# Performance work log

Hardware: AMD Instinct MI355X
Metric: run time of the kernel (lower is better)

The kernel has to match this reference:

```python
import jax, jax.numpy as jnp
import numpy as np

B, D, H = 4096, 1024, 1024


def setup_inputs() -> dict:
    key = jax.random.key(0)
    ks = jax.random.split(key, 20)
    s_in = 1.0 / np.sqrt(D)
    s_hid = 1.0 / np.sqrt(H)
    inp = {
        "x_t": jax.random.normal(ks[0], (B, D), dtype=jnp.float32),
        "h_t_1": jax.random.normal(ks[1], (B, H), dtype=jnp.float32),
        "c_t_1": jax.random.normal(ks[2], (B, H), dtype=jnp.float32),
        # input-to-hidden weights (nn.Linear: y = x @ W.T + b), stacked i,f,o,z
        "W": jax.random.uniform(ks[3], (4, H, D), minval=-s_in, maxval=s_in, dtype=jnp.float32),
        "bW": jax.random.uniform(ks[4], (4, H), minval=-s_in, maxval=s_in, dtype=jnp.float32),
        # hidden-to-hidden weights, stacked i,f,o,z
        "U": jax.random.uniform(ks[5], (4, H, H), minval=-s_hid, maxval=s_hid, dtype=jnp.float32),
        "bU": jax.random.uniform(ks[6], (4, H), minval=-s_hid, maxval=s_hid, dtype=jnp.float32),
    }
    return inp


def reference(x_t, h_t_1, c_t_1, W, bW, U, bU):
    # Two stacked GEMMs: [B,D]x[4,H,D] -> [4,B,H], [B,H]x[4,H,H] -> [4,B,H]
    gx = jnp.einsum("bd,ghd->gbh", x_t, W) + bW[:, None, :]
    gh = jnp.einsum("bh,gkh->gbk", h_t_1, U) + bU[:, None, :]
    g = gx + gh  # [4, B, H] pre-activations for i, f, o, z
    i = jax.nn.sigmoid(g[0])
    f = jax.nn.sigmoid(g[1])
    o = jax.nn.sigmoid(g[2])
    z = jnp.tanh(g[3])
    c_t = i * z + f * c_t_1
    h_t = o * jnp.tanh(c_t)
    return (h_t, c_t)
```

## Files before the change

kernel.cpp:

```cpp
#include <hip/hip_runtime.h>
#include <math.h>

#define Mm 4096
#define Nn 4096
#define Kk 2048

typedef __bf16 bf16x8 __attribute__((ext_vector_type(8)));
typedef float f32x4 __attribute__((ext_vector_type(4)));

__device__ __forceinline__ unsigned short f2bf(float f) {
    union { float f; unsigned u; } v; v.f = f;
    unsigned r = v.u + 0x7FFFu + ((v.u >> 16) & 1u);
    return (unsigned short)(r >> 16);
}

__device__ __forceinline__ float fast_tanh(float x) {
    return 1.f - 2.f / (1.f + __expf(2.f * x));
}

__global__ void pack_bf16(const float* __restrict__ x, const float* __restrict__ h,
                          const float* __restrict__ W, const float* __restrict__ U,
                          const float* __restrict__ bW, const float* __restrict__ bU,
                          unsigned short* __restrict__ Xc, unsigned short* __restrict__ Wc,
                          float* __restrict__ bsum) {
    if (blockIdx.x == 0) {
#pragma unroll
        for (int j = 0; j < 16; ++j) {
            int n = threadIdx.x * 16 + j;
            int hh = n >> 2, g = n & 3;
            bsum[n] = bW[g * 1024 + hh] + bU[g * 1024 + hh];
        }
    }
    const int PER = (4096 * 1024) / 4;
    for (int t = blockIdx.x * blockDim.x + threadIdx.x; t < 4 * PER;
         t += gridDim.x * blockDim.x) {
        int region = t >> 20;
        int i = t & (PER - 1);
        int row = i >> 8;
        int c4  = i & 255;
        const float* src = (region == 0) ? x : (region == 1) ? h : (region == 2) ? W : U;
        float4 v = reinterpret_cast<const float4*>(src)[i];
        ushort4 o;
        o.x = f2bf(v.x); o.y = f2bf(v.y); o.z = f2bf(v.z); o.w = f2bf(v.w);
        if (region < 2) {
            *reinterpret_cast<ushort4*>(Xc + (size_t)row * 2048 + (region << 10) + c4 * 4) = o;
        } else {
            int g = row >> 10, hh = row & 1023;
            int np = ((hh >> 4) << 6) + (g << 4) + (hh & 15);
            *reinterpret_cast<ushort4*>(Wc + (size_t)np * 2048 + ((region & 1) << 10) + c4 * 4) = o;
        }
    }
}

__device__ __forceinline__ void gl16(const void* g, void* l) {
    __builtin_amdgcn_global_load_lds(
        (const __attribute__((address_space(1))) void*)g,
        (__attribute__((address_space(3))) void*)l, 16, 0, 0);
}

#define A_OFF(p, ah) (((p) * 2 + (ah)) * 16384)
#define B_OFF(p, hb) (65536 + ((p) * 2 + (hb)) * 16384)

__global__ __launch_bounds__(512, 2) void gemm_8ph(const unsigned short* __restrict__ A,
                                                   const unsigned short* __restrict__ Bw,
                                                   const float* __restrict__ bsum,
                                                   const float* __restrict__ cprev,
                                                   float* __restrict__ out) {
    extern __shared__ char lds[];
    const int tid = threadIdx.x, lane = tid & 63, wave = tid >> 6;
    const int wm = wave >> 2, wn = wave & 3;

    const int bid = blockIdx.x;
    const int swz = (bid & 7) * 32 + (bid >> 3);
    const int bm = swz & 15, bn = swz >> 4;
    const size_t Crow0 = (size_t)bm * 256, Ccol0 = (size_t)bn * 256;

    const int srow = wave * 8 + (lane >> 3);
    const int scolswz = (((lane & 7) ^ (lane >> 3)) << 4);
    const char* aS[2][2];
    const char* bS[2][2];
#pragma unroll
    for (int ah = 0; ah < 2; ++ah)
#pragma unroll
        for (int j = 0; j < 2; ++j) {
            aS[ah][j] = (const char*)A  + (size_t)(Crow0 + ah * 128 + j * 64 + srow) * 4096 + scolswz;
            bS[ah][j] = (const char*)Bw + (size_t)(Ccol0 + ah * 128 + j * 64 + srow) * 4096 + scolswz;
        }

#define STG_A(p, ah, kb) do { \
        gl16(aS[ah][0] + (kb), lds + A_OFF(p, ah) + wave * 1024); \
        gl16(aS[ah][1] + (kb), lds + A_OFF(p, ah) + 8192 + wave * 1024); } while (0)
#define STG_B(p, hb, kb) do { \
        gl16(bS[hb][0] + (kb), lds + B_OFF(p, hb) + wave * 1024); \
        gl16(bS[hb][1] + (kb), lds + B_OFF(p, hb) + 8192 + wave * 1024); } while (0)

    const int arowB = (wm * 64 + (lane & 15)) * 128;
    const int browB = ((wn & 1) * 64 + (lane & 15)) * 128;
    const int c0 = (((lane >> 4) << 4)) ^ ((lane & 7) << 4);
    const int c1 = (64 + ((lane >> 4) << 4)) ^ ((lane & 7) << 4);
    const int bhb = wn >> 1;

#define LDA(p, ah, mfl, ck) (*(const bf16x8*)(lds + A_OFF(p, ah) + arowB + (mfl) * 2048 + (ck)))
#define LDB(p, nf, ck)      (*(const bf16x8*)(lds + B_OFF(p, bhb) + browB + (nf) * 2048 + (ck)))

    f32x4 acc[2][4][4] = {};

#define MFMA(a, b, c) __builtin_amdgcn_mfma_f32_16x16x32_bf16(a, b, c, 0, 0, 0)
#define MF16(ah, mfA, mfB, p00, p01, p10, p11) \
    acc[ah][mfA][0] = MFMA(p00, b00, acc[ah][mfA][0]); \
    acc[ah][mfA][1] = MFMA(p00, b10, acc[ah][mfA][1]); \
    acc[ah][mfA][2] = MFMA(p00, b20, acc[ah][mfA][2]); \
    acc[ah][mfA][3] = MFMA(p00, b30, acc[ah][mfA][3]); \
    acc[ah][mfB][0] = MFMA(p10, b00, acc[ah][mfB][0]); \
    acc[ah][mfB][1] = MFMA(p10, b10, acc[ah][mfB][1]); \
    acc[ah][mfB][2] = MFMA(p10, b20, acc[ah][mfB][2]); \
    acc[ah][mfB][3] = MFMA(p10, b30, acc[ah][mfB][3]); \
    acc[ah][mfA][0] = MFMA(p01, b01, acc[ah][mfA][0]); \
    acc[ah][mfA][1] = MFMA(p01, b11, acc[ah][mfA][1]); \
    acc[ah][mfA][2] = MFMA(p01, b21, acc[ah][mfA][2]); \
    acc[ah][mfA][3] = MFMA(p01, b31, acc[ah][mfA][3]); \
    acc[ah][mfB][0] = MFMA(p11, b01, acc[ah][mfB][0]); \
    acc[ah][mfB][1] = MFMA(p11, b11, acc[ah][mfB][1]); \
    acc[ah][mfB][2] = MFMA(p11, b21, acc[ah][mfB][2]); \
    acc[ah][mfB][3] = MFMA(p11, b31, acc[ah][mfB][3]);

#define SGB0 __builtin_amdgcn_sched_barrier(0)
#define SBAR __builtin_amdgcn_s_barrier()

#define GROUP(p, kbA1, kbT2) \
    { \
         \
        bf16x8 b00 = LDB(p, 0, c0), b01 = LDB(p, 0, c1), b10 = LDB(p, 1, c0), b11 = LDB(p, 1, c1); \
        bf16x8 b20 = LDB(p, 2, c0), b21 = LDB(p, 2, c1), b30 = LDB(p, 3, c0), b31 = LDB(p, 3, c1); \
        bf16x8 a0 = LDA(p, 0, 0, c0), a1 = LDA(p, 0, 0, c1); \
        bf16x8 a2 = LDA(p, 0, 1, c0), a3 = LDA(p, 0, 1, c1); \
        bf16x8 n0 = LDA(p, 0, 2, c0), n1 = LDA(p, 0, 2, c1); \
        bf16x8 n2 = LDA(p, 0, 3, c0), n3 = LDA(p, 0, 3, c1); \
        STG_A((p) ^ 1, 1, kbA1); \
        asm volatile("s_waitcnt vmcnt(6)" ::: "memory"); \
        SGB0; \
        __builtin_amdgcn_s_setprio(1); \
        MF16(0, 0, 1, a0, a1, a2, a3) \
        __builtin_amdgcn_s_setprio(0); \
        SBAR; \
         \
        a0 = LDA(p, 1, 0, c0); a1 = LDA(p, 1, 0, c1); \
        a2 = LDA(p, 1, 1, c0); a3 = LDA(p, 1, 1, c1); \
        STG_B(p, 0, kbT2); \
        asm volatile("s_waitcnt vmcnt(6)" ::: "memory"); \
        SGB0; \
        __builtin_amdgcn_s_setprio(1); \
        MF16(0, 2, 3, n0, n1, n2, n3) \
        __builtin_amdgcn_s_setprio(0); \
        SBAR; \
         \
        n0 = LDA(p, 1, 2, c0); n1 = LDA(p, 1, 2, c1); \
        n2 = LDA(p, 1, 3, c0); n3 = LDA(p, 1, 3, c1); \
        STG_A(p, 0, kbT2); \
        asm volatile("s_waitcnt vmcnt(6)" ::: "memory"); \
        SGB0; \
        __builtin_amdgcn_s_setprio(1); \
        MF16(1, 0, 1, a0, a1, a2, a3) \
        __builtin_amdgcn_s_setprio(0); \
        SBAR; \
         \
        STG_B(p, 1, kbT2); \
        SGB0; \
        __builtin_amdgcn_s_setprio(1); \
        MF16(1, 2, 3, n0, n1, n2, n3) \
        __builtin_amdgcn_s_setprio(0); \
        SBAR; \
    }

    STG_B(0, 0, 0);
    STG_A(0, 0, 0);
    STG_B(0, 1, 0);
    STG_A(0, 1, 0);
    STG_B(1, 0, 128);
    STG_A(1, 0, 128);
    STG_B(1, 1, 128);
    asm volatile("s_waitcnt vmcnt(6)" ::: "memory");
    __builtin_amdgcn_s_barrier();

    for (int it = 0; it < 16; ++it) {
        const int t0 = 2 * it;
        const size_t kA1_0 = (size_t)(t0 + 1) * 128;
        const size_t kT2_0 = (t0 + 2 <= 31) ? (size_t)(t0 + 2) * 128 : 0;
        const size_t kA1_1 = kT2_0;
        const size_t kT2_1 = (t0 + 3 <= 31) ? (size_t)(t0 + 3) * 128 : 0;
        GROUP(0, kA1_0, kT2_0)
        GROUP(1, kA1_1, kT2_1)
    }

    const int hl = lane & 15;
    const int er0 = (lane >> 4) * 4;
    const int myh = (int)(Ccol0 >> 2) + wn * 16 + hl;
    const f32x4 bs = *(const f32x4*)(bsum + (size_t)myh * 4);

    float cp[2][4][4];
#pragma unroll
    for (int ah = 0; ah < 2; ++ah)
#pragma unroll
        for (int mf = 0; mf < 4; ++mf)
#pragma unroll
            for (int r = 0; r < 4; ++r)
                cp[ah][mf][r] = cprev[(size_t)(Crow0 + ah * 128 + wm * 64 + mf * 16 + er0 + r) * 1024 + myh];

#pragma unroll
    for (int ah = 0; ah < 2; ++ah)
#pragma unroll
        for (int mf = 0; mf < 4; ++mf)
#pragma unroll
            for (int r = 0; r < 4; ++r) {
                float gi = acc[ah][mf][0][r] + bs[0];
                float gf = acc[ah][mf][1][r] + bs[1];
                float go = acc[ah][mf][2][r] + bs[2];
                float gz = acc[ah][mf][3][r] + bs[3];
                float iv = 1.f / (1.f + __expf(-gi));
                float fv = 1.f / (1.f + __expf(-gf));
                float ov = 1.f / (1.f + __expf(-go));
                float zv = fast_tanh(gz);
                float cc = fmaf(iv, zv, fv * cp[ah][mf][r]);
                float hv = ov * fast_tanh(cc);
                const size_t oidx =
                    (size_t)(Crow0 + ah * 128 + wm * 64 + mf * 16 + er0 + r) * 1024 + myh;
                out[oidx] = hv;
                out[(1 << 22) + oidx] = cc;
            }

    asm volatile("s_waitcnt vmcnt(0)" ::: "memory");
}

extern "C" void kernel_launch(void* const* d_in, const int* in_sizes, int n_in,
                              void* d_out, int out_size, void* d_ws, size_t ws_size,
                              hipStream_t stream) {
    const float* x  = (const float*)d_in[0];
    const float* h  = (const float*)d_in[1];
    const float* c  = (const float*)d_in[2];
    const float* W  = (const float*)d_in[3];
    const float* bW = (const float*)d_in[4];
    const float* U  = (const float*)d_in[5];
    const float* bU = (const float*)d_in[6];
    float* out = (float*)d_out;

    char* ws = (char*)d_ws;
    unsigned short* Xc = (unsigned short*)ws;
    unsigned short* Wc = (unsigned short*)(ws + ((size_t)16 << 20));
    float* bsum = (float*)(ws + ((size_t)32 << 20));

    (void)hipFuncSetAttribute((const void*)gemm_8ph,
                              hipFuncAttributeMaxDynamicSharedMemorySize, 131072);

    hipLaunchKernelGGL(pack_bf16, dim3(2048), dim3(256), 0, stream,
                       x, h, W, U, bW, bU, Xc, Wc, bsum);
    hipLaunchKernelGGL(gemm_8ph, dim3(256), dim3(512), 131072, stream,
                       Xc, Wc, bsum, c, out);
}
```

Before: 83.95 us.

## Prefetch next stage's B fragments and first A fragments across LDS buffers

```diff
diff --git a/kernel.cpp b/kernel.cpp
--- a/kernel.cpp
+++ b/kernel.cpp
@@ -104,25 +104,27 @@
 #define LDB(p, nf, ck)      (*(const bf16x8*)(lds + B_OFF(p, bhb) + browB + (nf) * 2048 + (ck)))
 
     f32x4 acc[2][4][4] = {};
+    bf16x8 bb[2][8];
+    bf16x8 pa[4], pn[4], pm[4];
 
 #define MFMA(a, b, c) __builtin_amdgcn_mfma_f32_16x16x32_bf16(a, b, c, 0, 0, 0)
-#define MF16(ah, mfA, mfB, p00, p01, p10, p11) \
-    acc[ah][mfA][0] = MFMA(p00, b00, acc[ah][mfA][0]); \
-    acc[ah][mfA][1] = MFMA(p00, b10, acc[ah][mfA][1]); \
-    acc[ah][mfA][2] = MFMA(p00, b20, acc[ah][mfA][2]); \
-    acc[ah][mfA][3] = MFMA(p00, b30, acc[ah][mfA][3]); \
-    acc[ah][mfB][0] = MFMA(p10, b00, acc[ah][mfB][0]); \
-    acc[ah][mfB][1] = MFMA(p10, b10, acc[ah][mfB][1]); \
-    acc[ah][mfB][2] = MFMA(p10, b20, acc[ah][mfB][2]); \
-    acc[ah][mfB][3] = MFMA(p10, b30, acc[ah][mfB][3]); \
-    acc[ah][mfA][0] = MFMA(p01, b01, acc[ah][mfA][0]); \
-    acc[ah][mfA][1] = MFMA(p01, b11, acc[ah][mfA][1]); \
-    acc[ah][mfA][2] = MFMA(p01, b21, acc[ah][mfA][2]); \
-    acc[ah][mfA][3] = MFMA(p01, b31, acc[ah][mfA][3]); \
-    acc[ah][mfB][0] = MFMA(p11, b01, acc[ah][mfB][0]); \
-    acc[ah][mfB][1] = MFMA(p11, b11, acc[ah][mfB][1]); \
-    acc[ah][mfB][2] = MFMA(p11, b21, acc[ah][mfB][2]); \
-    acc[ah][mfB][3] = MFMA(p11, b31, acc[ah][mfB][3]);
+#define MF16(ah, mfA, mfB, q, A0_, A1_, A2_, A3_) \
+    acc[ah][mfA][0] = MFMA(A0_, bb[q][0], acc[ah][mfA][0]); \
+    acc[ah][mfA][1] = MFMA(A0_, bb[q][2], acc[ah][mfA][1]); \
+    acc[ah][mfA][2] = MFMA(A0_, bb[q][4], acc[ah][mfA][2]); \
+    acc[ah][mfA][3] = MFMA(A0_, bb[q][6], acc[ah][mfA][3]); \
+    acc[ah][mfB][0] = MFMA(A2_, bb[q][0], acc[ah][mfB][0]); \
+    acc[ah][mfB][1] = MFMA(A2_, bb[q][2], acc[ah][mfB][1]); \
+    acc[ah][mfB][2] = MFMA(A2_, bb[q][4], acc[ah][mfB][2]); \
+    acc[ah][mfB][3] = MFMA(A2_, bb[q][6], acc[ah][mfB][3]); \
+    acc[ah][mfA][0] = MFMA(A1_, bb[q][1], acc[ah][mfA][0]); \
+    acc[ah][mfA][1] = MFMA(A1_, bb[q][3], acc[ah][mfA][1]); \
+    acc[ah][mfA][2] = MFMA(A1_, bb[q][5], acc[ah][mfA][2]); \
+    acc[ah][mfA][3] = MFMA(A1_, bb[q][7], acc[ah][mfA][3]); \
+    acc[ah][mfB][0] = MFMA(A3_, bb[q][1], acc[ah][mfB][0]); \
+    acc[ah][mfB][1] = MFMA(A3_, bb[q][3], acc[ah][mfB][1]); \
+    acc[ah][mfB][2] = MFMA(A3_, bb[q][5], acc[ah][mfB][2]); \
+    acc[ah][mfB][3] = MFMA(A3_, bb[q][7], acc[ah][mfB][3]);
 
 #define SGB0 __builtin_amdgcn_sched_barrier(0)
 #define SBAR __builtin_amdgcn_s_barrier()
@@ -130,44 +132,46 @@
 #define GROUP(p, kbA1, kbT2) \
     { \
          \
-        bf16x8 b00 = LDB(p, 0, c0), b01 = LDB(p, 0, c1), b10 = LDB(p, 1, c0), b11 = LDB(p, 1, c1); \
-        bf16x8 b20 = LDB(p, 2, c0), b21 = LDB(p, 2, c1), b30 = LDB(p, 3, c0), b31 = LDB(p, 3, c1); \
-        bf16x8 a0 = LDA(p, 0, 0, c0), a1 = LDA(p, 0, 0, c1); \
-        bf16x8 a2 = LDA(p, 0, 1, c0), a3 = LDA(p, 0, 1, c1); \
-        bf16x8 n0 = LDA(p, 0, 2, c0), n1 = LDA(p, 0, 2, c1); \
-        bf16x8 n2 = LDA(p, 0, 3, c0), n3 = LDA(p, 0, 3, c1); \
+        pa[0] = LDA(p, 0, 2, c0); pa[1] = LDA(p, 0, 2, c1); \
+        pa[2] = LDA(p, 0, 3, c0); pa[3] = LDA(p, 0, 3, c1); \
         STG_A((p) ^ 1, 1, kbA1); \
         asm volatile("s_waitcnt vmcnt(6)" ::: "memory"); \
         SGB0; \
         __builtin_amdgcn_s_setprio(1); \
-        MF16(0, 0, 1, a0, a1, a2, a3) \
-        __builtin_amdgcn_s_setprio(0); \
-        SBAR; \
-         \
-        a0 = LDA(p, 1, 0, c0); a1 = LDA(p, 1, 0, c1); \
-        a2 = LDA(p, 1, 1, c0); a3 = LDA(p, 1, 1, c1); \
+        MF16(0, 0, 1, p, pm[0], pm[1], pm[2], pm[3]) \
+        __builtin_amdgcn_s_setprio(0); \
+        SBAR; \
+         \
+        pn[0] = LDA(p, 1, 0, c0); pn[1] = LDA(p, 1, 0, c1); \
+        pn[2] = LDA(p, 1, 1, c0); pn[3] = LDA(p, 1, 1, c1); \
         STG_B(p, 0, kbT2); \
         asm volatile("s_waitcnt vmcnt(6)" ::: "memory"); \
         SGB0; \
         __builtin_amdgcn_s_setprio(1); \
-        MF16(0, 2, 3, n0, n1, n2, n3) \
-        __builtin_amdgcn_s_setprio(0); \
-        SBAR; \
-         \
-        n0 = LDA(p, 1, 2, c0); n1 = LDA(p, 1, 2, c1); \
-        n2 = LDA(p, 1, 3, c0); n3 = LDA(p, 1, 3, c1); \
+        MF16(0, 2, 3, p, pa[0], pa[1], pa[2], pa[3]) \
+        __builtin_amdgcn_s_setprio(0); \
+        SBAR; \
+         \
+        pa[0] = LDA(p, 1, 2, c0); pa[1] = LDA(p, 1, 2, c1); \
+        pa[2] = LDA(p, 1, 3, c0); pa[3] = LDA(p, 1, 3, c1); \
+        pm[0] = LDA((p) ^ 1, 0, 0, c0); pm[1] = LDA((p) ^ 1, 0, 0, c1); \
+        pm[2] = LDA((p) ^ 1, 0, 1, c0); pm[3] = LDA((p) ^ 1, 0, 1, c1); \
         STG_A(p, 0, kbT2); \
         asm volatile("s_waitcnt vmcnt(6)" ::: "memory"); \
         SGB0; \
         __builtin_amdgcn_s_setprio(1); \
-        MF16(1, 0, 1, a0, a1, a2, a3) \
-        __builtin_amdgcn_s_setprio(0); \
-        SBAR; \
-         \
+        MF16(1, 0, 1, p, pn[0], pn[1], pn[2], pn[3]) \
+        __builtin_amdgcn_s_setprio(0); \
+        SBAR; \
+         \
+        bb[(p) ^ 1][0] = LDB((p) ^ 1, 0, c0); bb[(p) ^ 1][1] = LDB((p) ^ 1, 0, c1); \
+        bb[(p) ^ 1][2] = LDB((p) ^ 1, 1, c0); bb[(p) ^ 1][3] = LDB((p) ^ 1, 1, c1); \
+        bb[(p) ^ 1][4] = LDB((p) ^ 1, 2, c0); bb[(p) ^ 1][5] = LDB((p) ^ 1, 2, c1); \
+        bb[(p) ^ 1][6] = LDB((p) ^ 1, 3, c0); bb[(p) ^ 1][7] = LDB((p) ^ 1, 3, c1); \
         STG_B(p, 1, kbT2); \
         SGB0; \
         __builtin_amdgcn_s_setprio(1); \
-        MF16(1, 2, 3, n0, n1, n2, n3) \
+        MF16(1, 2, 3, p, pa[0], pa[1], pa[2], pa[3]) \
         __builtin_amdgcn_s_setprio(0); \
         SBAR; \
     }
@@ -181,6 +185,12 @@
     STG_B(1, 1, 128);
     asm volatile("s_waitcnt vmcnt(6)" ::: "memory");
     __builtin_amdgcn_s_barrier();
+    bb[0][0] = LDB(0, 0, c0); bb[0][1] = LDB(0, 0, c1);
+    bb[0][2] = LDB(0, 1, c0); bb[0][3] = LDB(0, 1, c1);
+    bb[0][4] = LDB(0, 2, c0); bb[0][5] = LDB(0, 2, c1);
+    bb[0][6] = LDB(0, 3, c0); bb[0][7] = LDB(0, 3, c1);
+    pm[0] = LDA(0, 0, 0, c0); pm[1] = LDA(0, 0, 0, c1);
+    pm[2] = LDA(0, 0, 1, c0); pm[3] = LDA(0, 0, 1, c1);
 
     for (int it = 0; it < 16; ++it) {
         const int t0 = 2 * it;
```

After: 107.2 us. +27.7%, slower.
